# Optimization experiments

Hardware: AMD Instinct MI355X
Metric: run time of the kernel (lower is better)

Reference implementation:

```python
import jax, jax.numpy as jnp
import numpy as np

B = 64          # graphs per batch
N_PER = 1024    # nodes per graph
N = B * N_PER   # 65536 total nodes
E_PER = 8192    # edges per graph (sorted by graph)
E = B * E_PER   # 524288 total edges
HID = 256       # config.model.dim_hidden
RATIO = 0.5     # causal_ratio
N_RES = int(RATIO * E_PER)  # edges kept per graph (n_reserve)


def setup_inputs() -> dict:
    key = jax.random.key(0)
    ks = jax.random.split(key, 12)
    x = jax.random.normal(ks[0], (N, HID), jnp.float32)
    # per-graph edges, no self-loops, sorted by graph id (split_batch assumption)
    base = jnp.repeat(jnp.arange(B, dtype=jnp.int32) * N_PER, E_PER)
    row_loc = jax.random.randint(ks[1], (E,), 0, N_PER, dtype=jnp.int32)
    off = jax.random.randint(ks[2], (E,), 1, N_PER, dtype=jnp.int32)
    col_loc = (row_loc + off) % N_PER
    edge_index = jnp.stack([base + row_loc, base + col_loc])  # [2, E]
    batch = jnp.repeat(jnp.arange(B, dtype=jnp.int32), N_PER)  # [N]

    def lin(k, fan_in, shape):
        return (jax.random.normal(k, shape, jnp.float32) / np.sqrt(fan_in)).astype(jnp.float32)

    # 2-layer GIN MLP params (eps = 0)
    W11 = lin(ks[3], HID, (HID, HID)); b11 = jnp.zeros((HID,), jnp.float32)
    W12 = lin(ks[4], HID, (HID, HID)); b12 = jnp.zeros((HID,), jnp.float32)
    W21 = lin(ks[5], HID, (HID, HID)); b21 = jnp.zeros((HID,), jnp.float32)
    W22 = lin(ks[6], HID, (HID, HID)); b22 = jnp.zeros((HID,), jnp.float32)
    # edge scoring linear: Linear(2*HID, 1)
    w_score = lin(ks[7], 2 * HID, (2 * HID,))
    b_score = jnp.zeros((), jnp.float32)
    return {"x": x, "edge_index": edge_index, "batch": batch,
            "W11": W11, "b11": b11, "W12": W12, "b12": b12,
            "W21": W21, "b21": b21, "W22": W22, "b22": b22,
            "w_score": w_score, "b_score": b_score}


def _gin_layer(h, row, col, W1, b1, W2, b2):
    agg = jax.ops.segment_sum(h[col], row, num_segments=N)  # sum over in-edges
    h = h + agg  # (1 + eps) * x + aggregate, eps = 0
    h = jax.nn.relu(h @ W1 + b1)
    return jax.nn.relu(h @ W2 + b2)


def _relabel(h, batch, ei_sub):
    # torch: sub_nodes = unique(edge_index); compact + remap. Padded to N for fixed shapes.
    sub = jnp.unique(ei_sub, size=N, fill_value=N)  # [N], padded with sentinel N
    node_idx = jnp.zeros((N + 1,), jnp.int32).at[sub].set(jnp.arange(N, dtype=jnp.int32))
    h_pad = jnp.concatenate([h, jnp.zeros((1, h.shape[1]), h.dtype)], axis=0)
    b_pad = jnp.concatenate([batch, jnp.full((1,), -1, batch.dtype)], axis=0)
    return h_pad[sub], node_idx[ei_sub], b_pad[sub]


def reference(x, edge_index, batch, W11, b11, W12, b12, W21, b21, W22, b22, w_score, b_score):
    row, col = edge_index[0], edge_index[1]
    h = _gin_layer(x, row, col, W11, b11, W12, b12)
    h = _gin_layer(h, row, col, W21, b21, W22, b22)  # [N, HID]

    # edge_score = Linear(cat(h[row], h[col])) without materializing [E, 2*HID]
    s_src = h @ w_score[:HID]   # [N]
    s_dst = h @ w_score[HID:]   # [N]
    edge_score = s_src[row] + s_dst[col] + b_score  # [E]

    # per-graph sort-based top-k split (split_graph), batched over B graphs
    s = edge_score.reshape(B, E_PER)
    rank = jnp.argsort(-s, axis=1)                      # descending
    idx_res, idx_drop = rank[:, :N_RES], rank[:, N_RES:]
    ei = edge_index.reshape(2, B, E_PER)

    def gather_edges(idx):
        return jnp.take_along_axis(ei, jnp.broadcast_to(idx[None], (2, B, idx.shape[1])), axis=2).reshape(2, -1)

    causal_ei = gather_edges(idx_res)
    conf_ei = gather_edges(idx_drop)
    causal_w = jnp.take_along_axis(s, idx_res, axis=1).reshape(-1)
    conf_w = -jnp.take_along_axis(s, idx_drop, axis=1).reshape(-1)

    causal_x, causal_ei_rel, causal_batch = _relabel(h, batch, causal_ei)
    conf_x, conf_ei_rel, conf_batch = _relabel(h, batch, conf_ei)

    return (causal_x, causal_ei_rel, causal_w, causal_batch,
            conf_x, conf_ei_rel, conf_w, conf_batch, edge_score)
```

## Files before the change

### kernel.cpp

```cpp
#include <hip/hip_runtime.h>
#include <hip/hip_bf16.h>

#define NN      65536
#define EE      524288
#define HIDC    256
#define BB      64
#define EPB     8192
#define NPB     1024
#define NRES    4096

#define O_CX    0
#define O_CEI   16777216
#define O_CW    17301504
#define O_CB    17563648
#define O_FX    17629184
#define O_FEI   34406400
#define O_FW    34930688
#define O_FB    35192832
#define O_ES    35258368

typedef __attribute__((ext_vector_type(8))) short short8v;
typedef __attribute__((ext_vector_type(4))) float f32x4;

__device__ __forceinline__ unsigned f2ord(float f) {
    unsigned u = __float_as_uint(f);
    return (u & 0x80000000u) ? ~u : (u | 0x80000000u);
}

__device__ __forceinline__ unsigned packsplit(float v) {
    unsigned u = __float_as_uint(v);
    unsigned hi = (u + 0x7FFFu + ((u >> 16) & 1u)) & 0xFFFF0000u;
    float lo = v - __uint_as_float(hi);
    unsigned ul = __float_as_uint(lo);
    unsigned lo16 = (ul + 0x7FFFu + ((ul >> 16) & 1u)) >> 16;
    return hi | lo16;
}

__global__ void k_init(int* __restrict__ flagC, int* __restrict__ flagF) {
    int v = blockIdx.x * blockDim.x + threadIdx.x;
    if (v < NN) { flagC[v] = 0; flagF[v] = 0; }
}

__global__ void k_wsplit(const float* __restrict__ W11, const float* __restrict__ W12,
                         const float* __restrict__ W21, const float* __restrict__ W22,
                         unsigned* __restrict__ Wtp) {
    int g = blockIdx.x * 256 + threadIdx.x;
    int w = g >> 16, r = g & 65535;
    int n = r >> 8, k = r & 255;
    const float* W = (w == 0) ? W11 : (w == 1) ? W12 : (w == 2) ? W21 : W22;
    Wtp[g] = packsplit(W[k * 256 + n]);
}

__global__ __launch_bounds__(1024) void k_sort_csr(const int* __restrict__ row,
                                                   int* __restrict__ sortedKey) {
    __shared__ unsigned lds[EPB];
    int b = blockIdx.x, t = threadIdx.x;
    int base = b * EPB;
    for (int i = t; i < EPB; i += 1024) {
        int r = row[base + i] & (NPB - 1);
        lds[i] = ((unsigned)r << 13) | (unsigned)i;
    }
    __syncthreads();
    for (int k = 2; k <= EPB; k <<= 1) {
        for (int j = k >> 1; j > 0; j >>= 1) {
            for (int t2 = t; t2 < EPB / 2; t2 += 1024) {
                int i = ((t2 & ~(j - 1)) << 1) | (t2 & (j - 1));
                int l = i | j;
                unsigned a = lds[i], c = lds[l];
                bool up = ((i & k) == 0);
                if ((a > c) == up) { lds[i] = c; lds[l] = a; }
            }
            __syncthreads();
        }
    }
    for (int i = t; i < EPB; i += 1024) sortedKey[base + i] = (int)lds[i];
}

__global__ void k_rowptr(const int* __restrict__ sortedKey, int* __restrict__ rowPtr) {
    int v = blockIdx.x * blockDim.x + threadIdx.x;
    if (v >= NN) return;
    int b = v >> 10, r = v & (NPB - 1);
    const int* keys = sortedKey + b * EPB;
    int target = r << 13;
    int lo = 0, hi = EPB;
    while (lo < hi) { int mid = (lo + hi) >> 1; if (keys[mid] < target) lo = mid + 1; else hi = mid; }
    rowPtr[v] = b * EPB + lo;
    if (v == 0) rowPtr[NN] = EE;
}

__global__ void k_colgather(const int* __restrict__ sortedKey, const int* __restrict__ col,
                            int* __restrict__ colSorted) {
    int g = blockIdx.x * 256 + threadIdx.x;
    int b = g >> 13;
    int le = sortedKey[g] & (EPB - 1);
    colSorted[g] = col[(b << 13) | le];
}

__global__ __launch_bounds__(256) void k_agg(const float* __restrict__ src,
                                             const float* __restrict__ resid,
                                             const int* __restrict__ colSorted,
                                             const int* __restrict__ rowPtr,
                                             unsigned* __restrict__ dstP) {
    int lane = threadIdx.x & 63;
    int v = blockIdx.x * 4 + (threadIdx.x >> 6);
    int e0 = rowPtr[v], e1 = rowPtr[v + 1];
    int cnt = e1 - e0;
    float4 acc = make_float4(0.f, 0.f, 0.f, 0.f);
    int myc = (lane < cnt) ? colSorted[e0 + lane] : 0;
    int lim = cnt < 64 ? cnt : 64;
    for (int base = 0; base < lim; base += 8) {
        int n = lim - base; if (n > 8) n = 8;
        float4 tv[8];
#pragma unroll
        for (int j = 0; j < 8; ++j)
            if (j < n) {
                int c = __shfl(myc, base + j, 64);
                tv[j] = *((const float4*)src + (size_t)c * 64 + lane);
            }
#pragma unroll
        for (int j = 0; j < 8; ++j)
            if (j < n) { acc.x += tv[j].x; acc.y += tv[j].y; acc.z += tv[j].z; acc.w += tv[j].w; }
    }
    for (int e = e0 + 64; e < e1; ++e) {
        int c = colSorted[e];
        float4 sv = *((const float4*)src + (size_t)c * 64 + lane);
        acc.x += sv.x; acc.y += sv.y; acc.z += sv.z; acc.w += sv.w;
    }
    float4 rv = *((const float4*)resid + (size_t)v * 64 + lane);
    uint4 o;
    o.x = packsplit(rv.x + acc.x);
    o.y = packsplit(rv.y + acc.y);
    o.z = packsplit(rv.z + acc.z);
    o.w = packsplit(rv.w + acc.w);
    *((uint4*)dstP + (size_t)v * 64 + lane) = o;
}

template<int EPI>
__global__ __launch_bounds__(256) void k_gemm_mfma(const unsigned* __restrict__ Ap,
                                                   const unsigned* __restrict__ Wtp,
                                                   const float* __restrict__ bias,
                                                   void* __restrict__ Cout) {
    __shared__ short Ah[128][40];
    __shared__ short Al[128][40];
    __shared__ short Bh[128][40];
    __shared__ short Bl[128][40];
    int t = threadIdx.x;
    int lane = t & 63, wave = t >> 6;
    int bm = blockIdx.x * 128, bn = blockIdx.y * 128;
    int ln = lane & 15, qd = lane >> 4;
    f32x4 acc[2][8];
#pragma unroll
    for (int i = 0; i < 2; ++i)
#pragma unroll
        for (int j = 0; j < 8; ++j) acc[i][j] = (f32x4){0.f, 0.f, 0.f, 0.f};
    int row = t >> 1, half = t & 1;
    const uint4* ag = (const uint4*)(Ap + (size_t)(bm + row) * 256) + half * 4;
    const uint4* bg = (const uint4*)(Wtp + (size_t)(bn + row) * 256) + half * 4;
    for (int k0 = 0; k0 < 256; k0 += 32) {
        uint4 av[4], bv[4];
#pragma unroll
        for (int s = 0; s < 4; ++s) { av[s] = ag[s]; bv[s] = bg[s]; }
        ag += 8; bg += 8;
        __syncthreads();
#pragma unroll
        for (int s = 0; s < 4; ++s) {
            int kc = half * 16 + s * 4;
            *(short4*)&Ah[row][kc] = make_short4((short)(av[s].x >> 16), (short)(av[s].y >> 16),
                                                 (short)(av[s].z >> 16), (short)(av[s].w >> 16));
            *(short4*)&Al[row][kc] = make_short4((short)av[s].x, (short)av[s].y,
                                                 (short)av[s].z, (short)av[s].w);
            *(short4*)&Bh[row][kc] = make_short4((short)(bv[s].x >> 16), (short)(bv[s].y >> 16),
                                                 (short)(bv[s].z >> 16), (short)(bv[s].w >> 16));
            *(short4*)&Bl[row][kc] = make_short4((short)bv[s].x, (short)bv[s].y,
                                                 (short)bv[s].z, (short)bv[s].w);
        }
        __syncthreads();
        short8v ah0 = *(short8v*)&Ah[wave * 32 + ln][qd * 8];
        short8v ah1 = *(short8v*)&Ah[wave * 32 + 16 + ln][qd * 8];
        short8v al0 = *(short8v*)&Al[wave * 32 + ln][qd * 8];
        short8v al1 = *(short8v*)&Al[wave * 32 + 16 + ln][qd * 8];
#pragma unroll
        for (int nt = 0; nt < 8; ++nt) {
            short8v bh = *(short8v*)&Bh[nt * 16 + ln][qd * 8];
            short8v bl = *(short8v*)&Bl[nt * 16 + ln][qd * 8];
            f32x4 c0 = acc[0][nt];
            c0 = __builtin_amdgcn_mfma_f32_16x16x32_bf16(al0, bl, c0, 0, 0, 0);
            c0 = __builtin_amdgcn_mfma_f32_16x16x32_bf16(al0, bh, c0, 0, 0, 0);
            c0 = __builtin_amdgcn_mfma_f32_16x16x32_bf16(ah0, bl, c0, 0, 0, 0);
            c0 = __builtin_amdgcn_mfma_f32_16x16x32_bf16(ah0, bh, c0, 0, 0, 0);
            acc[0][nt] = c0;
            f32x4 c1 = acc[1][nt];
            c1 = __builtin_amdgcn_mfma_f32_16x16x32_bf16(al1, bl, c1, 0, 0, 0);
            c1 = __builtin_amdgcn_mfma_f32_16x16x32_bf16(al1, bh, c1, 0, 0, 0);
            c1 = __builtin_amdgcn_mfma_f32_16x16x32_bf16(ah1, bl, c1, 0, 0, 0);
            c1 = __builtin_amdgcn_mfma_f32_16x16x32_bf16(ah1, bh, c1, 0, 0, 0);
            acc[1][nt] = c1;
        }
    }
#pragma unroll
    for (int nt = 0; nt < 8; ++nt) {
        float bvs = bias[bn + nt * 16 + ln];
#pragma unroll
        for (int mt = 0; mt < 2; ++mt)
#pragma unroll
            for (int r = 0; r < 4; ++r) {
                int gm = bm + wave * 32 + mt * 16 + qd * 4 + r;
                int gn = bn + nt * 16 + ln;
                float v = acc[mt][nt][r] + bvs;
                v = v > 0.f ? v : 0.f;
                if (EPI == 0) ((unsigned*)Cout)[(size_t)gm * 256 + gn] = packsplit(v);
                else          ((float*)Cout)[(size_t)gm * 256 + gn] = v;
            }
    }
}

__global__ __launch_bounds__(256) void k_score(const float* __restrict__ h,
                                               const float* __restrict__ wsc,
                                               float* __restrict__ sSrc,
                                               float* __restrict__ sDst) {
    int wave = threadIdx.x >> 6, lane = threadIdx.x & 63;
    int v = blockIdx.x * 4 + wave;
    int c0 = lane << 2;
    float4 hv = *(const float4*)(h + (size_t)v * HIDC + c0);
    float4 w0 = *(const float4*)(wsc + c0);
    float4 w1 = *(const float4*)(wsc + HIDC + c0);
    float p0 = (hv.x * w0.x + hv.y * w0.y) + (hv.z * w0.z + hv.w * w0.w);
    float p1 = (hv.x * w1.x + hv.y * w1.y) + (hv.z * w1.z + hv.w * w1.w);
#pragma unroll
    for (int off = 32; off > 0; off >>= 1) {
        p0 += __shfl_down(p0, off, 64);
        p1 += __shfl_down(p1, off, 64);
    }
    if (lane == 0) { sSrc[v] = p0; sDst[v] = p1; }
}

__global__ void k_escore(const int* __restrict__ row, const int* __restrict__ col,
                         const float* __restrict__ sSrc, const float* __restrict__ sDst,
                         const float* __restrict__ bsc, float* __restrict__ out9) {
    int e = blockIdx.x * blockDim.x + threadIdx.x;
    if (e >= EE) return;
    out9[e] = sSrc[row[e]] + sDst[col[e]] + bsc[0];
}

__global__ __launch_bounds__(1024) void k_sort_scores(const float* __restrict__ esc,
                                                      int* __restrict__ perm) {
    __shared__ unsigned long long lds[EPB];
    int b = blockIdx.x, t = threadIdx.x;
    int base = b * EPB;
    for (int i = t; i < EPB; i += 1024) {
        unsigned m = f2ord(esc[base + i]);
        lds[i] = ((unsigned long long)(~m) << 32) | (unsigned)i;
    }
    __syncthreads();
    for (int k = 2; k <= EPB; k <<= 1) {
        for (int j = k >> 1; j > 0; j >>= 1) {
            for (int t2 = t; t2 < EPB / 2; t2 += 1024) {
                int i = ((t2 & ~(j - 1)) << 1) | (t2 & (j - 1));
                int l = i | j;
                unsigned long long a = lds[i], c = lds[l];
                bool up = ((i & k) == 0);
                if ((a > c) == up) { lds[i] = c; lds[l] = a; }
            }
            __syncthreads();
        }
    }
    for (int i = t; i < EPB; i += 1024) perm[base + i] = (int)(lds[i] & 0x1FFFull);
}

__global__ void k_flags(const int* __restrict__ perm, const int* __restrict__ row,
                        const int* __restrict__ col, const float* __restrict__ esc,
                        int* __restrict__ flagC, int* __restrict__ flagF,
                        float* __restrict__ outCW, float* __restrict__ outFW) {
    int g = blockIdx.x * blockDim.x + threadIdx.x;
    if (g >= EE) return;
    int b = g >> 13, jj = g & (EPB - 1);
    int ge = (b << 13) | perm[g];
    int r = row[ge], c = col[ge];
    float s = esc[ge];
    if (jj < NRES) {
        flagC[r] = 1; flagC[c] = 1;
        outCW[b * NRES + jj] = s;
    } else {
        flagF[r] = 1; flagF[c] = 1;
        outFW[b * NRES + (jj - NRES)] = -s;
    }
}

__global__ __launch_bounds__(256) void k_scan1(const int* __restrict__ fc, const int* __restrict__ ff,
                                               int* __restrict__ bsC, int* __restrict__ bsF) {
    __shared__ int s1[256], s2[256];
    int t = threadIdx.x, v = blockIdx.x * 256 + t;
    s1[t] = fc[v]; s2[t] = ff[v];
    __syncthreads();
    for (int off = 128; off > 0; off >>= 1) {
        if (t < off) { s1[t] += s1[t + off]; s2[t] += s2[t + off]; }
        __syncthreads();
    }
    if (t == 0) { bsC[blockIdx.x] = s1[0]; bsF[blockIdx.x] = s2[0]; }
}

__global__ __launch_bounds__(256) void k_scan2(const int* __restrict__ bsC, const int* __restrict__ bsF,
                                               int* __restrict__ boC, int* __restrict__ boF,
                                               int* __restrict__ prefC, int* __restrict__ prefF) {
    __shared__ int s1[256], s2[256];
    int t = threadIdx.x;
    int v1 = bsC[t], v2 = bsF[t];
    s1[t] = v1; s2[t] = v2;
    __syncthreads();
    for (int off = 1; off < 256; off <<= 1) {
        int a1 = (t >= off) ? s1[t - off] : 0;
        int a2 = (t >= off) ? s2[t - off] : 0;
        __syncthreads();
        s1[t] += a1; s2[t] += a2;
        __syncthreads();
    }
    boC[t] = s1[t] - v1; boF[t] = s2[t] - v2;
    if (t == 255) { prefC[NN] = s1[255]; prefF[NN] = s2[255]; }
}

__global__ __launch_bounds__(256) void k_scan3(const int* __restrict__ fc, const int* __restrict__ ff,
                                               const int* __restrict__ boC, const int* __restrict__ boF,
                                               int* __restrict__ prefC, int* __restrict__ prefF) {
    __shared__ int s1[256], s2[256];
    int t = threadIdx.x, v = blockIdx.x * 256 + t;
    int f1 = fc[v], f2 = ff[v];
    s1[t] = f1; s2[t] = f2;
    __syncthreads();
    for (int off = 1; off < 256; off <<= 1) {
        int a1 = (t >= off) ? s1[t - off] : 0;
        int a2 = (t >= off) ? s2[t - off] : 0;
        __syncthreads();
        s1[t] += a1; s2[t] += a2;
        __syncthreads();
    }
    prefC[v] = boC[blockIdx.x] + s1[t] - f1;
    prefF[v] = boF[blockIdx.x] + s2[t] - f2;
}

__global__ __launch_bounds__(256) void k_scatter(const int* __restrict__ flag, const int* __restrict__ pref,
                                                 const float* __restrict__ h,
                                                 float* __restrict__ outX, float* __restrict__ outB) {
    int wave = threadIdx.x >> 6, lane = threadIdx.x & 63;
    int i = blockIdx.x * 4 + wave;
    int c0 = lane << 2;
    int nu = pref[NN];
    if (flag[i]) {
        int pos = pref[i];
        *(float4*)(outX + (size_t)pos * HIDC + c0) = *(const float4*)(h + (size_t)i * HIDC + c0);
        if (lane == 0) outB[pos] = (float)(i >> 10);
    }
    if (i >= nu) {
        float4 z = make_float4(0.f, 0.f, 0.f, 0.f);
        *(float4*)(outX + (size_t)i * HIDC + c0) = z;
        if (lane == 0) outB[i] = -1.0f;
    }
}

__global__ void k_eirel(const int* __restrict__ perm, const int* __restrict__ row,
                        const int* __restrict__ col, const int* __restrict__ prefC,
                        const int* __restrict__ prefF,
                        float* __restrict__ outC, float* __restrict__ outF) {
    int g = blockIdx.x * blockDim.x + threadIdx.x;
    if (g >= EE) return;
    int b = g >> 13, jj = g & (EPB - 1);
    int ge = (b << 13) | perm[g];
    int r = row[ge], c = col[ge];
    if (jj < NRES) {
        int idx = b * NRES + jj;
        outC[idx] = (float)prefC[r];
        outC[BB * NRES + idx] = (float)prefC[c];
    } else {
        int idx = b * NRES + (jj - NRES);
        outF[idx] = (float)prefF[r];
        outF[BB * NRES + idx] = (float)prefF[c];
    }
}

extern "C" void kernel_launch(void* const* d_in, const int* in_sizes, int n_in,
                              void* d_out, int out_size, void* d_ws, size_t ws_size,
                              hipStream_t stream) {
    const float* x   = (const float*)d_in[0];
    const int*   ei  = (const int*)d_in[1];
    const int*   row = ei;
    const int*   col = ei + EE;
    const float* W11 = (const float*)d_in[3];
    const float* b11 = (const float*)d_in[4];
    const float* W12 = (const float*)d_in[5];
    const float* b12 = (const float*)d_in[6];
    const float* W21 = (const float*)d_in[7];
    const float* b21 = (const float*)d_in[8];
    const float* W22 = (const float*)d_in[9];
    const float* b22 = (const float*)d_in[10];
    const float* wsc = (const float*)d_in[11];
    const float* bsc = (const float*)d_in[12];

    float* out = (float*)d_out;

    void* X = (void*)(out + O_CX);

    char* w = (char*)d_ws;
    auto alloc = [&](size_t bytes) { char* p = w; w += (bytes + 255) & ~(size_t)255; return p; };
    void*  P         = (void*)alloc((size_t)NN * HIDC * 4);
    float* sSrc      = (float*)alloc((size_t)NN * 4);
    float* sDst      = (float*)alloc((size_t)NN * 4);
    int*   sortedKey = (int*)alloc((size_t)EE * 4);
    int*   colSorted = (int*)alloc((size_t)EE * 4);
    int*   rowPtr    = (int*)alloc((size_t)(NN + 1) * 4);
    int*   perm      = (int*)alloc((size_t)EE * 4);
    int*   flagC     = (int*)alloc((size_t)NN * 4);
    int*   flagF     = (int*)alloc((size_t)NN * 4);
    int*   prefC     = (int*)alloc((size_t)(NN + 1) * 4);
    int*   prefF     = (int*)alloc((size_t)(NN + 1) * 4);
    unsigned* Wtp    = (unsigned*)alloc((size_t)4 * 65536 * 4);
    int*   bsC       = (int*)alloc(256 * 4);
    int*   bsF       = (int*)alloc(256 * 4);
    int*   boC       = (int*)alloc(256 * 4);
    int*   boF       = (int*)alloc(256 * 4);

    float* esc = out + O_ES;

    hipLaunchKernelGGL(k_init, dim3(NN / 256), dim3(256), 0, stream, flagC, flagF);
    hipLaunchKernelGGL(k_wsplit, dim3(1024), dim3(256), 0, stream, W11, W12, W21, W22, Wtp);
    hipLaunchKernelGGL(k_sort_csr, dim3(BB), dim3(1024), 0, stream, row, sortedKey);
    hipLaunchKernelGGL(k_rowptr, dim3(NN / 256), dim3(256), 0, stream, sortedKey, rowPtr);
    hipLaunchKernelGGL(k_colgather, dim3(EE / 256), dim3(256), 0, stream, sortedKey, col, colSorted);

    dim3 ggrid(NN / 128, 2), gblk(256);

    hipLaunchKernelGGL(k_agg, dim3(NN / 4), dim3(256), 0, stream, x, x, colSorted, rowPtr, (unsigned*)X);
    k_gemm_mfma<0><<<ggrid, gblk, 0, stream>>>((const unsigned*)X, Wtp + 0 * 65536, b11, P);
    k_gemm_mfma<1><<<ggrid, gblk, 0, stream>>>((const unsigned*)P, Wtp + 1 * 65536, b12, X);
    hipLaunchKernelGGL(k_agg, dim3(NN / 4), dim3(256), 0, stream, (const float*)X, (const float*)X,
                       colSorted, rowPtr, (unsigned*)P);
    k_gemm_mfma<0><<<ggrid, gblk, 0, stream>>>((const unsigned*)P, Wtp + 2 * 65536, b21, X);
    k_gemm_mfma<1><<<ggrid, gblk, 0, stream>>>((const unsigned*)X, Wtp + 3 * 65536, b22, P);

    const float* h = (const float*)P;

    hipLaunchKernelGGL(k_score, dim3(NN / 4), dim3(256), 0, stream, h, wsc, sSrc, sDst);
    hipLaunchKernelGGL(k_escore, dim3(EE / 256), dim3(256), 0, stream, row, col, sSrc, sDst, bsc, esc);

    hipLaunchKernelGGL(k_sort_scores, dim3(BB), dim3(1024), 0, stream, esc, perm);
    hipLaunchKernelGGL(k_flags, dim3(EE / 256), dim3(256), 0, stream, perm, row, col, esc,
                       flagC, flagF, out + O_CW, out + O_FW);

    hipLaunchKernelGGL(k_scan1, dim3(NN / 256), dim3(256), 0, stream, flagC, flagF, bsC, bsF);
    hipLaunchKernelGGL(k_scan2, dim3(1), dim3(256), 0, stream, bsC, bsF, boC, boF, prefC, prefF);
    hipLaunchKernelGGL(k_scan3, dim3(NN / 256), dim3(256), 0, stream, flagC, flagF, boC, boF, prefC, prefF);

    hipLaunchKernelGGL(k_scatter, dim3(NN / 4), dim3(256), 0, stream, flagC, prefC, h,
                       out + O_CX, out + O_CB);
    hipLaunchKernelGGL(k_scatter, dim3(NN / 4), dim3(256), 0, stream, flagF, prefF, h,
                       out + O_FX, out + O_FB);
    hipLaunchKernelGGL(k_eirel, dim3(EE / 256), dim3(256), 0, stream, perm, row, col,
                       prefC, prefF, out + O_CEI, out + O_FEI);
}
```

Measured before the change: 714.2 us.

## Replace CSR sort with counting sort, fuse scoring into GEMM, split score sort

Builds the CSR with a per-graph histogram and atomic counting sort in place of a bitonic sort, a binary search and a gather. It folds the edge-score dot products into the last GEMM epilogue using shuffles and atomics, and drops the low-by-low MFMA term of the split-bf16 product. It also splits the per-graph score sort into two half-sorts plus a merge pass across 128 blocks, fusing the flag writes into the final stage, and merges the two scatter launches into one. Risks: the CSR column order within a row is no longer deterministic, and removing the lo*lo term slightly lowers GEMM precision.

Measured after the change: 622.7 us. -12.8%, faster.

```diff
diff --git a/kernel.cpp b/kernel.cpp
--- a/kernel.cpp
+++ b/kernel.cpp
@@ -36,9 +36,10 @@
     return hi | lo16;
 }
 
-__global__ void k_init(int* __restrict__ flagC, int* __restrict__ flagF) {
+__global__ void k_init(int* __restrict__ flagC, int* __restrict__ flagF,
+                       float* __restrict__ sSrc, float* __restrict__ sDst) {
     int v = blockIdx.x * blockDim.x + threadIdx.x;
-    if (v < NN) { flagC[v] = 0; flagF[v] = 0; }
+    if (v < NN) { flagC[v] = 0; flagF[v] = 0; sSrc[v] = 0.f; sDst[v] = 0.f; }
 }
 
 __global__ void k_wsplit(const float* __restrict__ W11, const float* __restrict__ W12,
@@ -51,49 +52,44 @@
     Wtp[g] = packsplit(W[k * 256 + n]);
 }
 
-__global__ __launch_bounds__(1024) void k_sort_csr(const int* __restrict__ row,
-                                                   int* __restrict__ sortedKey) {
-    __shared__ unsigned lds[EPB];
+__global__ __launch_bounds__(1024) void k_csr(const int* __restrict__ row,
+                                              const int* __restrict__ col,
+                                              int* __restrict__ rowPtr,
+                                              int* __restrict__ colSorted) {
+    __shared__ int hist[NPB];
+    __shared__ int scn[NPB];
     int b = blockIdx.x, t = threadIdx.x;
     int base = b * EPB;
-    for (int i = t; i < EPB; i += 1024) {
-        int r = row[base + i] & (NPB - 1);
-        lds[i] = ((unsigned)r << 13) | (unsigned)i;
-    }
-    __syncthreads();
-    for (int k = 2; k <= EPB; k <<= 1) {
-        for (int j = k >> 1; j > 0; j >>= 1) {
-            for (int t2 = t; t2 < EPB / 2; t2 += 1024) {
-                int i = ((t2 & ~(j - 1)) << 1) | (t2 & (j - 1));
-                int l = i | j;
-                unsigned a = lds[i], c = lds[l];
-                bool up = ((i & k) == 0);
-                if ((a > c) == up) { lds[i] = c; lds[l] = a; }
-            }
-            __syncthreads();
-        }
-    }
-    for (int i = t; i < EPB; i += 1024) sortedKey[base + i] = (int)lds[i];
-}
-
-__global__ void k_rowptr(const int* __restrict__ sortedKey, int* __restrict__ rowPtr) {
-    int v = blockIdx.x * blockDim.x + threadIdx.x;
-    if (v >= NN) return;
-    int b = v >> 10, r = v & (NPB - 1);
-    const int* keys = sortedKey + b * EPB;
-    int target = r << 13;
-    int lo = 0, hi = EPB;
-    while (lo < hi) { int mid = (lo + hi) >> 1; if (keys[mid] < target) lo = mid + 1; else hi = mid; }
-    rowPtr[v] = b * EPB + lo;
-    if (v == 0) rowPtr[NN] = EE;
-}
-
-__global__ void k_colgather(const int* __restrict__ sortedKey, const int* __restrict__ col,
-                            int* __restrict__ colSorted) {
-    int g = blockIdx.x * 256 + threadIdx.x;
-    int b = g >> 13;
-    int le = sortedKey[g] & (EPB - 1);
-    colSorted[g] = col[(b << 13) | le];
+    hist[t] = 0;
+    __syncthreads();
+    int r[8], c[8];
+#pragma unroll
+    for (int j = 0; j < 8; ++j) {
+        int e = base + t + j * 1024;
+        r[j] = row[e] & (NPB - 1);
+        c[j] = col[e];
+        atomicAdd(&hist[r[j]], 1);
+    }
+    __syncthreads();
+    int v = hist[t];
+    scn[t] = v;
+    __syncthreads();
+    for (int off = 1; off < 1024; off <<= 1) {
+        int a = (t >= off) ? scn[t - off] : 0;
+        __syncthreads();
+        scn[t] += a;
+        __syncthreads();
+    }
+    int start = scn[t] - v;
+    rowPtr[b * NPB + t] = base + start;
+    if (b == 0 && t == 0) rowPtr[NN] = EE;
+    hist[t] = start;
+    __syncthreads();
+#pragma unroll
+    for (int j = 0; j < 8; ++j) {
+        int pos = atomicAdd(&hist[r[j]], 1);
+        colSorted[base + pos] = c[j];
+    }
 }
 
 __global__ __launch_bounds__(256) void k_agg(const float* __restrict__ src,
@@ -135,11 +131,14 @@
     *((uint4*)dstP + (size_t)v * 64 + lane) = o;
 }
 
-template<int EPI>
+template<int EPI, int SC>
 __global__ __launch_bounds__(256) void k_gemm_mfma(const unsigned* __restrict__ Ap,
                                                    const unsigned* __restrict__ Wtp,
                                                    const float* __restrict__ bias,
-                                                   void* __restrict__ Cout) {
+                                                   void* __restrict__ Cout,
+                                                   const float* __restrict__ wsc,
+                                                   float* __restrict__ sSrc,
+                                                   float* __restrict__ sDst) {
     __shared__ short Ah[128][40];
     __shared__ short Al[128][40];
     __shared__ short Bh[128][40];
@@ -184,22 +183,23 @@
             short8v bh = *(short8v*)&Bh[nt * 16 + ln][qd * 8];
             short8v bl = *(short8v*)&Bl[nt * 16 + ln][qd * 8];
             f32x4 c0 = acc[0][nt];
-            c0 = __builtin_amdgcn_mfma_f32_16x16x32_bf16(al0, bl, c0, 0, 0, 0);
             c0 = __builtin_amdgcn_mfma_f32_16x16x32_bf16(al0, bh, c0, 0, 0, 0);
             c0 = __builtin_amdgcn_mfma_f32_16x16x32_bf16(ah0, bl, c0, 0, 0, 0);
             c0 = __builtin_amdgcn_mfma_f32_16x16x32_bf16(ah0, bh, c0, 0, 0, 0);
             acc[0][nt] = c0;
             f32x4 c1 = acc[1][nt];
-            c1 = __builtin_amdgcn_mfma_f32_16x16x32_bf16(al1, bl, c1, 0, 0, 0);
             c1 = __builtin_amdgcn_mfma_f32_16x16x32_bf16(al1, bh, c1, 0, 0, 0);
             c1 = __builtin_amdgcn_mfma_f32_16x16x32_bf16(ah1, bl, c1, 0, 0, 0);
             c1 = __builtin_amdgcn_mfma_f32_16x16x32_bf16(ah1, bh, c1, 0, 0, 0);
             acc[1][nt] = c1;
         }
     }
+    float ps[2][4] = {}, pd[2][4] = {};
 #pragma unroll
     for (int nt = 0; nt < 8; ++nt) {
         float bvs = bias[bn + nt * 16 + ln];
+        float ws = 0.f, wd = 0.f;
+        if (SC) { ws = wsc[bn + nt * 16 + ln]; wd = wsc[256 + bn + nt * 16 + ln]; }
 #pragma unroll
         for (int mt = 0; mt < 2; ++mt)
 #pragma unroll
@@ -208,30 +208,32 @@
                 int gn = bn + nt * 16 + ln;
                 float v = acc[mt][nt][r] + bvs;
                 v = v > 0.f ? v : 0.f;
+                if (SC) { ps[mt][r] += v * ws; pd[mt][r] += v * wd; }
                 if (EPI == 0) ((unsigned*)Cout)[(size_t)gm * 256 + gn] = packsplit(v);
                 else          ((float*)Cout)[(size_t)gm * 256 + gn] = v;
             }
     }
-}
-
-__global__ __launch_bounds__(256) void k_score(const float* __restrict__ h,
-                                               const float* __restrict__ wsc,
-                                               float* __restrict__ sSrc,
-                                               float* __restrict__ sDst) {
-    int wave = threadIdx.x >> 6, lane = threadIdx.x & 63;
-    int v = blockIdx.x * 4 + wave;
-    int c0 = lane << 2;
-    float4 hv = *(const float4*)(h + (size_t)v * HIDC + c0);
-    float4 w0 = *(const float4*)(wsc + c0);
-    float4 w1 = *(const float4*)(wsc + HIDC + c0);
-    float p0 = (hv.x * w0.x + hv.y * w0.y) + (hv.z * w0.z + hv.w * w0.w);
-    float p1 = (hv.x * w1.x + hv.y * w1.y) + (hv.z * w1.z + hv.w * w1.w);
-#pragma unroll
-    for (int off = 32; off > 0; off >>= 1) {
-        p0 += __shfl_down(p0, off, 64);
-        p1 += __shfl_down(p1, off, 64);
-    }
-    if (lane == 0) { sSrc[v] = p0; sDst[v] = p1; }
+    if (SC) {
+#pragma unroll
+        for (int off = 1; off < 16; off <<= 1)
+#pragma unroll
+            for (int mt = 0; mt < 2; ++mt)
+#pragma unroll
+                for (int r = 0; r < 4; ++r) {
+                    ps[mt][r] += __shfl_xor(ps[mt][r], off, 64);
+                    pd[mt][r] += __shfl_xor(pd[mt][r], off, 64);
+                }
+        if (ln == 0) {
+#pragma unroll
+            for (int mt = 0; mt < 2; ++mt)
+#pragma unroll
+                for (int r = 0; r < 4; ++r) {
+                    int gm = bm + wave * 32 + mt * 16 + qd * 4 + r;
+                    atomicAdd(&sSrc[gm], ps[mt][r]);
+                    atomicAdd(&sDst[gm], pd[mt][r]);
+                }
+        }
+    }
 }
 
 __global__ void k_escore(const int* __restrict__ row, const int* __restrict__ col,
@@ -242,47 +244,71 @@
     out9[e] = sSrc[row[e]] + sDst[col[e]] + bsc[0];
 }
 
-__global__ __launch_bounds__(1024) void k_sort_scores(const float* __restrict__ esc,
-                                                      int* __restrict__ perm) {
-    __shared__ unsigned long long lds[EPB];
-    int b = blockIdx.x, t = threadIdx.x;
-    int base = b * EPB;
-    for (int i = t; i < EPB; i += 1024) {
-        unsigned m = f2ord(esc[base + i]);
-        lds[i] = ((unsigned long long)(~m) << 32) | (unsigned)i;
-    }
-    __syncthreads();
-    for (int k = 2; k <= EPB; k <<= 1) {
+__global__ __launch_bounds__(512) void k_sortS1(const float* __restrict__ esc,
+                                                unsigned long long* __restrict__ keys) {
+    __shared__ unsigned long long lds[4096];
+    int blk = blockIdx.x, b = blk >> 1, c = blk & 1;
+    int t = threadIdx.x;
+    int gbase = b * EPB + c * 4096;
+    for (int i = t; i < 4096; i += 512) {
+        int idx = c * 4096 + i;
+        unsigned m = f2ord(esc[b * EPB + idx]);
+        lds[i] = ((unsigned long long)(~m) << 32) | (unsigned)idx;
+    }
+    __syncthreads();
+    bool dirbit = (c != 0);
+    for (int k = 2; k <= 4096; k <<= 1) {
         for (int j = k >> 1; j > 0; j >>= 1) {
-            for (int t2 = t; t2 < EPB / 2; t2 += 1024) {
+            for (int t2 = t; t2 < 2048; t2 += 512) {
                 int i = ((t2 & ~(j - 1)) << 1) | (t2 & (j - 1));
                 int l = i | j;
-                unsigned long long a = lds[i], c = lds[l];
-                bool up = ((i & k) == 0);
-                if ((a > c) == up) { lds[i] = c; lds[l] = a; }
+                unsigned long long a = lds[i], d = lds[l];
+                bool up = (((i & k) == 0) != dirbit);
+                if ((a > d) == up) { lds[i] = d; lds[l] = a; }
             }
             __syncthreads();
         }
     }
-    for (int i = t; i < EPB; i += 1024) perm[base + i] = (int)(lds[i] & 0x1FFFull);
-}
-
-__global__ void k_flags(const int* __restrict__ perm, const int* __restrict__ row,
-                        const int* __restrict__ col, const float* __restrict__ esc,
-                        int* __restrict__ flagC, int* __restrict__ flagF,
-                        float* __restrict__ outCW, float* __restrict__ outFW) {
-    int g = blockIdx.x * blockDim.x + threadIdx.x;
-    if (g >= EE) return;
-    int b = g >> 13, jj = g & (EPB - 1);
-    int ge = (b << 13) | perm[g];
-    int r = row[ge], c = col[ge];
-    float s = esc[ge];
-    if (jj < NRES) {
-        flagC[r] = 1; flagC[c] = 1;
-        outCW[b * NRES + jj] = s;
-    } else {
-        flagF[r] = 1; flagF[c] = 1;
-        outFW[b * NRES + (jj - NRES)] = -s;
+    for (int i = t; i < 4096; i += 512) keys[gbase + i] = lds[i];
+}
+
+__global__ void k_sortS2(unsigned long long* __restrict__ keys) {
+    int g = blockIdx.x * 256 + threadIdx.x;
+    int b = g >> 12, i = g & 4095;
+    unsigned long long* p = keys + b * EPB;
+    unsigned long long a = p[i], d = p[i + 4096];
+    if (a > d) { p[i] = d; p[i + 4096] = a; }
+}
+
+__global__ __launch_bounds__(512) void k_sortS3(const unsigned long long* __restrict__ keys,
+                                                const int* __restrict__ row, const int* __restrict__ col,
+                                                const float* __restrict__ esc,
+                                                int* __restrict__ perm,
+                                                int* __restrict__ flagC, int* __restrict__ flagF,
+                                                float* __restrict__ outCW, float* __restrict__ outFW) {
+    __shared__ unsigned long long lds[4096];
+    int blk = blockIdx.x, b = blk >> 1, c = blk & 1;
+    int gbase = b * EPB + c * 4096;
+    int t = threadIdx.x;
+    for (int i = t; i < 4096; i += 512) lds[i] = keys[gbase + i];
+    __syncthreads();
+    for (int j = 2048; j > 0; j >>= 1) {
+        for (int t2 = t; t2 < 2048; t2 += 512) {
+            int i = ((t2 & ~(j - 1)) << 1) | (t2 & (j - 1));
+            int l = i | j;
+            unsigned long long a = lds[i], d = lds[l];
+            if (a > d) { lds[i] = d; lds[l] = a; }
+        }
+        __syncthreads();
+    }
+    for (int i = t; i < 4096; i += 512) {
+        int idx = (int)(lds[i] & 0x1FFFull);
+        int ge = b * EPB + idx;
+        perm[gbase + i] = idx;
+        int r = row[ge], cl = col[ge];
+        float s = esc[ge];
+        if (c == 0) { flagC[r] = 1; flagC[cl] = 1; outCW[b * NRES + i] = s; }
+        else        { flagF[r] = 1; flagF[cl] = 1; outFW[b * NRES + i] = -s; }
     }
 }
 
@@ -337,23 +363,31 @@
     prefF[v] = boF[blockIdx.x] + s2[t] - f2;
 }
 
-__global__ __launch_bounds__(256) void k_scatter(const int* __restrict__ flag, const int* __restrict__ pref,
-                                                 const float* __restrict__ h,
-                                                 float* __restrict__ outX, float* __restrict__ outB) {
-    int wave = threadIdx.x >> 6, lane = threadIdx.x & 63;
-    int i = blockIdx.x * 4 + wave;
+__global__ __launch_bounds__(256) void k_scatter2(const int* __restrict__ flagC, const int* __restrict__ prefC,
+                                                  const int* __restrict__ flagF, const int* __restrict__ prefF,
+                                                  const float* __restrict__ h,
+                                                  float* __restrict__ outCX, float* __restrict__ outCB,
+                                                  float* __restrict__ outFX, float* __restrict__ outFB) {
+    int lane = threadIdx.x & 63;
+    int i = blockIdx.x * 4 + (threadIdx.x >> 6);
     int c0 = lane << 2;
-    int nu = pref[NN];
-    if (flag[i]) {
-        int pos = pref[i];
-        *(float4*)(outX + (size_t)pos * HIDC + c0) = *(const float4*)(h + (size_t)i * HIDC + c0);
-        if (lane == 0) outB[pos] = (float)(i >> 10);
-    }
-    if (i >= nu) {
-        float4 z = make_float4(0.f, 0.f, 0.f, 0.f);
-        *(float4*)(outX + (size_t)i * HIDC + c0) = z;
-        if (lane == 0) outB[i] = -1.0f;
-    }
+    int fC = flagC[i], fF = flagF[i];
+    float4 hv = make_float4(0.f, 0.f, 0.f, 0.f);
+    if (fC | fF) hv = *(const float4*)(h + (size_t)i * HIDC + c0);
+    if (fC) {
+        int p = prefC[i];
+        *(float4*)(outCX + (size_t)p * HIDC + c0) = hv;
+        if (lane == 0) outCB[p] = (float)(i >> 10);
+    }
+    if (fF) {
+        int p = prefF[i];
+        *(float4*)(outFX + (size_t)p * HIDC + c0) = hv;
+        if (lane == 0) outFB[p] = (float)(i >> 10);
+    }
+    int nuC = prefC[NN], nuF = prefF[NN];
+    float4 z = make_float4(0.f, 0.f, 0.f, 0.f);
+    if (i >= nuC) { *(float4*)(outCX + (size_t)i * HIDC + c0) = z; if (lane == 0) outCB[i] = -1.0f; }
+    if (i >= nuF) { *(float4*)(outFX + (size_t)i * HIDC + c0) = z; if (lane == 0) outFB[i] = -1.0f; }
 }
 
 __global__ void k_eirel(const int* __restrict__ perm, const int* __restrict__ row,
@@ -403,10 +437,10 @@
     void*  P         = (void*)alloc((size_t)NN * HIDC * 4);
     float* sSrc      = (float*)alloc((size_t)NN * 4);
     float* sDst      = (float*)alloc((size_t)NN * 4);
-    int*   sortedKey = (int*)alloc((size_t)EE * 4);
     int*   colSorted = (int*)alloc((size_t)EE * 4);
     int*   rowPtr    = (int*)alloc((size_t)(NN + 1) * 4);
     int*   perm      = (int*)alloc((size_t)EE * 4);
+    unsigned long long* keys64 = (unsigned long long*)alloc((size_t)EE * 8);
     int*   flagC     = (int*)alloc((size_t)NN * 4);
     int*   flagF     = (int*)alloc((size_t)NN * 4);
     int*   prefC     = (int*)alloc((size_t)(NN + 1) * 4);
@@ -419,39 +453,39 @@
 
     float* esc = out + O_ES;
 
-    hipLaunchKernelGGL(k_init, dim3(NN / 256), dim3(256), 0, stream, flagC, flagF);
+    hipLaunchKernelGGL(k_init, dim3(NN / 256), dim3(256), 0, stream, flagC, flagF, sSrc, sDst);
     hipLaunchKernelGGL(k_wsplit, dim3(1024), dim3(256), 0, stream, W11, W12, W21, W22, Wtp);
-    hipLaunchKernelGGL(k_sort_csr, dim3(BB), dim3(1024), 0, stream, row, sortedKey);
-    hipLaunchKernelGGL(k_rowptr, dim3(NN / 256), dim3(256), 0, stream, sortedKey, rowPtr);
-    hipLaunchKernelGGL(k_colgather, dim3(EE / 256), dim3(256), 0, stream, sortedKey, col, colSorted);
+    hipLaunchKernelGGL(k_csr, dim3(BB), dim3(1024), 0, stream, row, col, rowPtr, colSorted);
 
     dim3 ggrid(NN / 128, 2), gblk(256);
 
     hipLaunchKernelGGL(k_agg, dim3(NN / 4), dim3(256), 0, stream, x, x, colSorted, rowPtr, (unsigned*)X);
-    k_gemm_mfma<0><<<ggrid, gblk, 0, stream>>>((const unsigned*)X, Wtp + 0 * 65536, b11, P);
-    k_gemm_mfma<1><<<ggrid, gblk, 0, stream>>>((const unsigned*)P, Wtp + 1 * 65536, b12, X);
+    k_gemm_mfma<0, 0><<<ggrid, gblk, 0, stream>>>((const unsigned*)X, Wtp + 0 * 65536, b11, P,
+                                                  nullptr, nullptr, nullptr);
+    k_gemm_mfma<1, 0><<<ggrid, gblk, 0, stream>>>((const unsigned*)P, Wtp + 1 * 65536, b12, X,
+                                                  nullptr, nullptr, nullptr);
     hipLaunchKernelGGL(k_agg, dim3(NN / 4), dim3(256), 0, stream, (const float*)X, (const float*)X,
                        colSorted, rowPtr, (unsigned*)P);
-    k_gemm_mfma<0><<<ggrid, gblk, 0, stream>>>((const unsigned*)P, Wtp + 2 * 65536, b21, X);
-    k_gemm_mfma<1><<<ggrid, gblk, 0, stream>>>((const unsigned*)X, Wtp + 3 * 65536, b22, P);
+    k_gemm_mfma<0, 0><<<ggrid, gblk, 0, stream>>>((const unsigned*)P, Wtp + 2 * 65536, b21, X,
+                                                  nullptr, nullptr, nullptr);
+    k_gemm_mfma<1, 1><<<ggrid, gblk, 0, stream>>>((const unsigned*)X, Wtp + 3 * 65536, b22, P,
+                                                  wsc, sSrc, sDst);
 
     const float* h = (const float*)P;
 
-    hipLaunchKernelGGL(k_score, dim3(NN / 4), dim3(256), 0, stream, h, wsc, sSrc, sDst);
     hipLaunchKernelGGL(k_escore, dim3(EE / 256), dim3(256), 0, stream, row, col, sSrc, sDst, bsc, esc);
 
-    hipLaunchKernelGGL(k_sort_scores, dim3(BB), dim3(1024), 0, stream, esc, perm);
-    hipLaunchKernelGGL(k_flags, dim3(EE / 256), dim3(256), 0, stream, perm, row, col, esc,
-                       flagC, flagF, out + O_CW, out + O_FW);
+    hipLaunchKernelGGL(k_sortS1, dim3(BB * 2), dim3(512), 0, stream, esc, keys64);
+    hipLaunchKernelGGL(k_sortS2, dim3(EE / 512), dim3(256), 0, stream, keys64);
+    hipLaunchKernelGGL(k_sortS3, dim3(BB * 2), dim3(512), 0, stream, keys64, row, col, esc,
+                       perm, flagC, flagF, out + O_CW, out + O_FW);
 
     hipLaunchKernelGGL(k_scan1, dim3(NN / 256), dim3(256), 0, stream, flagC, flagF, bsC, bsF);
     hipLaunchKernelGGL(k_scan2, dim3(1), dim3(256), 0, stream, bsC, bsF, boC, boF, prefC, prefF);
     hipLaunchKernelGGL(k_scan3, dim3(NN / 256), dim3(256), 0, stream, flagC, flagF, boC, boF, prefC, prefF);
 
-    hipLaunchKernelGGL(k_scatter, dim3(NN / 4), dim3(256), 0, stream, flagC, prefC, h,
-                       out + O_CX, out + O_CB);
-    hipLaunchKernelGGL(k_scatter, dim3(NN / 4), dim3(256), 0, stream, flagF, prefF, h,
-                       out + O_FX, out + O_FB);
+    hipLaunchKernelGGL(k_scatter2, dim3(NN / 4), dim3(256), 0, stream, flagC, prefC, flagF, prefF, h,
+                       out + O_CX, out + O_CB, out + O_FX, out + O_FB);
     hipLaunchKernelGGL(k_eirel, dim3(EE / 256), dim3(256), 0, stream, perm, row, col,
                        prefC, prefF, out + O_CEI, out + O_FEI);
 }
```
